# Optimization experiments

Measured on AMD Instinct MI355X. Metric: run time of the kernel, lower is better.

The kernel has to match this reference:

```python
import jax, jax.numpy as jnp
import numpy as np

NUM_GROUPS = 512   # G: number of FPS centers
GROUP_SIZE = 32    # K: neighbors per group


def setup_inputs() -> dict:
    key = jax.random.key(0)
    points = jax.random.normal(key, (16, 8192, 6), dtype=jnp.float32)  # [B,N,C], xyz = first 3 ch
    return {"points": points}


def _farthest_point_sampling(xyz, K):
    """Iterative FPS. xyz: [B,N,3] -> indices [B,K] (int32).

    Deterministic start at index 0 (the torch module uses a random start; we fix
    it for a reproducible reference -- the math per step is identical).
    """
    B, N, _ = xyz.shape
    start = jnp.zeros((B,), dtype=jnp.int32)
    min_d = jnp.full((B, N), jnp.inf, dtype=xyz.dtype)

    def step(carry, _):
        min_d, last = carry
        last_pt = jnp.take_along_axis(xyz, last[:, None, None], axis=1)  # [B,1,3]
        d = jnp.sum((xyz - last_pt) ** 2, axis=-1)                       # [B,N]
        min_d = jnp.minimum(min_d, d)
        nxt = jnp.argmax(min_d, axis=-1).astype(jnp.int32)
        return (min_d, nxt), last

    _, idxs = jax.lax.scan(step, (min_d, start), None, length=K)
    return jnp.transpose(idxs)  # [B,K]


def reference(points):
    xyz = points[:, :, :3]                                   # [B,N,3]
    fps_idx = _farthest_point_sampling(xyz, NUM_GROUPS)      # [B,G]
    centers = jnp.take_along_axis(xyz, fps_idx[:, :, None], axis=1)  # [B,G,3]

    # Squared pairwise distances [B,G,N] via expanded GEMM (compute-dominant part).
    d2 = (jnp.sum(centers * centers, axis=-1)[:, :, None]
          - 2.0 * jnp.einsum('bgc,bnc->bgn', centers, xyz)
          + jnp.sum(xyz * xyz, axis=-1)[:, None, :])

    # KNN: smallest K distances (torch uses return_sorted=False; ordering of the
    # K neighbors is irrelevant to the grouping semantics).
    _, knn_idx = jax.lax.top_k(-d2, GROUP_SIZE)              # [B,G,K]

    # knn_gather: [B,N,C] gathered by [B,G,K] -> [B,G,K,C]
    grouped = jax.vmap(lambda p, i: p[i])(points, knn_idx)

    # Center-subtract on xyz channels only.
    grouped = jnp.concatenate(
        [grouped[..., :3] - centers[:, :, None, :], grouped[..., 3:]], axis=-1)
    return grouped, centers
```

## Files before the change

### kernel.cpp

```cpp
#include <hip/hip_runtime.h>
#include <hip/hip_bf16.h>
#include <stdint.h>

#define BATCH 16
#define NPTS  8192
#define NCH   6
#define NGRP  512
#define GSZ   32

#define TPB    1024
#define FPS_PPT 8
#define FPS_W   16
#define GPB     4
#define KNB     (BATCH * NGRP / GPB)

typedef float v2f __attribute__((ext_vector_type(2)));

template <int CTRL>
__device__ __forceinline__ float dpp_max_f32(float v) {
  const int t =
      __builtin_amdgcn_update_dpp(0, __float_as_int(v), CTRL, 0xf, 0xf, true);
  return fmaxf(v, __int_as_float(t));
}

template <int CTRL>
__device__ __forceinline__ unsigned dpp_min_u32(unsigned v) {
  const int t = __builtin_amdgcn_update_dpp((int)0xFFFFFFFF, (int)v, CTRL,
                                            0xf, 0xf, false);
  const unsigned tu = (unsigned)t;
  return v < tu ? v : tu;
}

__global__ __launch_bounds__(TPB, 1) void fused_kernel(
    const float* __restrict__ points, float* __restrict__ grouped,
    float* __restrict__ centers, unsigned* __restrict__ ws) {
#pragma clang fp contract(off)
  __shared__ union {
    struct {
      float cache[NPTS * 3];
      unsigned long long wdata[2][FPS_W];
      unsigned wtag[2][FPS_W];
    } f;
    struct {
      unsigned long long wtop[16][GSZ];
      int knn_sh[GPB][GSZ];
    } k;
  } u;
  __shared__ unsigned ticket_sh;

  const int tid  = threadIdx.x;
  const int lane = tid & 63;
  const int wave = tid >> 6;

  if (tid == 0) ticket_sh = atomicAdd(ws, 1u);
  __syncthreads();
  const unsigned ticket = ticket_sh;

  if (ticket < BATCH) {
    const int b = (int)ticket;
    const float* P = points + (size_t)b * NPTS * NCH;
    float* C = centers + (size_t)b * NGRP * 3;
    unsigned* prog = ws + 32 + b * 32;

    v2f px[4], py[4], pz[4], md[4];
    {
      float* fx = (float*)px; float* fy = (float*)py; float* fz = (float*)pz;
#pragma unroll
      for (int j = 0; j < FPS_PPT; ++j) {
        const int i = tid * FPS_PPT + j;
        const float x = P[i * 6 + 0];
        const float y = P[i * 6 + 1];
        const float z = P[i * 6 + 2];
        fx[j] = x; fy[j] = y; fz[j] = z;
        u.f.cache[i * 3 + 0] = x;
        u.f.cache[i * 3 + 1] = y;
        u.f.cache[i * 3 + 2] = z;
      }
#pragma unroll
      for (int j = 0; j < 4; ++j)
        md[j] = (v2f){__builtin_inff(), __builtin_inff()};
    }
    if (tid < 32) u.f.wtag[tid >> 4][tid & 15] = 0;
    __syncthreads();

    float lx = u.f.cache[0], ly = u.f.cache[1], lz = u.f.cache[2];

    for (int k = 1; k < NGRP; ++k) {
      if (tid == 0) {
        if ((k & 7) == 0)
          __hip_atomic_store(prog, (unsigned)(k - 1), __ATOMIC_RELEASE,
                             __HIP_MEMORY_SCOPE_AGENT);
        C[(k - 1) * 3 + 0] = lx;
        C[(k - 1) * 3 + 1] = ly;
        C[(k - 1) * 3 + 2] = lz;
      }

      const v2f vlx = {lx, lx}, vly = {ly, ly}, vlz = {lz, lz};
      v2f b2 = {-__builtin_inff(), -__builtin_inff()};
#pragma unroll
      for (int j = 0; j < 4; ++j) {
        const v2f dx = px[j] - vlx;
        const v2f dy = py[j] - vly;
        const v2f dz = pz[j] - vlz;
        const v2f d  = (dx * dx + dy * dy) + dz * dz;
        md[j] = __builtin_elementwise_min(md[j], d);
        b2 = __builtin_elementwise_max(b2, md[j]);
      }
      const float bestv = fmaxf(b2.x, b2.y);

      unsigned idxbest = 0;
#pragma unroll
      for (int j = 3; j >= 0; --j) {
        idxbest = (md[j].y == bestv) ? (unsigned)(tid * 8 + 2 * j + 1) : idxbest;
        idxbest = (md[j].x == bestv) ? (unsigned)(tid * 8 + 2 * j)     : idxbest;
      }

      float wv = bestv;
      wv = dpp_max_f32<0x111>(wv); wv = dpp_max_f32<0x112>(wv);
      wv = dpp_max_f32<0x114>(wv); wv = dpp_max_f32<0x118>(wv);
      wv = dpp_max_f32<0x142>(wv); wv = dpp_max_f32<0x143>(wv);
      const float wvmax =
          __int_as_float(__builtin_amdgcn_readlane(__float_as_int(wv), 63));
      const int owner = (int)__builtin_ctzll(__ballot(bestv == wvmax));

      const int p = k & 1;
      if (lane == owner) {
        __hip_atomic_store(&u.f.wdata[p][wave],
                           ((unsigned long long)__float_as_uint(wvmax) << 32) |
                               idxbest,
                           __ATOMIC_RELAXED, __HIP_MEMORY_SCOPE_WORKGROUP);
        __hip_atomic_store(&u.f.wtag[p][wave], (unsigned)k, __ATOMIC_RELEASE,
                           __HIP_MEMORY_SCOPE_WORKGROUP);
      }

      unsigned tg;
      do {
        tg = __hip_atomic_load(&u.f.wtag[p][lane & 15], __ATOMIC_ACQUIRE,
                               __HIP_MEMORY_SCOPE_WORKGROUP);
      } while (__ballot(tg == (unsigned)k) != ~0ull);

      const unsigned long long slot =
          __hip_atomic_load(&u.f.wdata[p][lane & 15], __ATOMIC_RELAXED,
                            __HIP_MEMORY_SCOPE_WORKGROUP);
      const unsigned sidx = (unsigned)(slot & 0xFFFFFFFFull);
      const float    sval = __uint_as_float((unsigned)(slot >> 32));
      const float ccx = u.f.cache[sidx * 3 + 0];
      const float ccy = u.f.cache[sidx * 3 + 1];
      const float ccz = u.f.cache[sidx * 3 + 2];

      float r = sval;
      r = dpp_max_f32<0x111>(r); r = dpp_max_f32<0x112>(r);
      r = dpp_max_f32<0x114>(r); r = dpp_max_f32<0x118>(r);
      const float gmax =
          __int_as_float(__builtin_amdgcn_readlane(__float_as_int(r), 15));
      const int sstar =
          (int)__builtin_ctzll(__ballot(sval == gmax) & 0xFFFFull);
      lx = __int_as_float(__builtin_amdgcn_readlane(__float_as_int(ccx), sstar));
      ly = __int_as_float(__builtin_amdgcn_readlane(__float_as_int(ccy), sstar));
      lz = __int_as_float(__builtin_amdgcn_readlane(__float_as_int(ccz), sstar));
    }
    if (tid == 0) {
      C[(NGRP - 1) * 3 + 0] = lx;
      C[(NGRP - 1) * 3 + 1] = ly;
      C[(NGRP - 1) * 3 + 2] = lz;
      __hip_atomic_store(prog, (unsigned)NGRP, __ATOMIC_RELEASE,
                         __HIP_MEMORY_SCOPE_AGENT);
    }
  } else {
    const unsigned gid = ticket - BATCH;
    const int b  = (int)(gid & 15);
    const int g0 = (int)(gid >> 4) * GPB;
    const int sub  = tid >> 8;
    const int t256 = tid & 255;
    const int g = g0 + sub;
    const float* P = points + (size_t)b * NPTS * NCH;
    const float* cen = centers + ((size_t)b * NGRP + g) * 3;
    unsigned* prog = ws + 32 + b * 32;

    if (tid == 0) {
      while (__hip_atomic_load(prog, __ATOMIC_ACQUIRE,
                               __HIP_MEMORY_SCOPE_AGENT) <
             (unsigned)(g0 + GPB))
        __builtin_amdgcn_s_sleep(64);
    }
    __syncthreads();

    const float cx = __hip_atomic_load(&cen[0], __ATOMIC_RELAXED,
                                       __HIP_MEMORY_SCOPE_AGENT);
    const float cy = __hip_atomic_load(&cen[1], __ATOMIC_RELAXED,
                                       __HIP_MEMORY_SCOPE_AGENT);
    const float cz = __hip_atomic_load(&cen[2], __ATOMIC_RELAXED,
                                       __HIP_MEMORY_SCOPE_AGENT);
    const float cc = (cx * cx + cy * cy) + cz * cz;

    unsigned long long keys[32];
#pragma unroll
    for (int j = 0; j < 32; ++j) {
      const int i = j * 256 + t256;
      const float2 xy = *reinterpret_cast<const float2*>(P + (size_t)i * 6);
      const float x = xy.x, y = xy.y;
      const float z = P[i * 6 + 2];
      const float xx  = (x * x + y * y) + z * z;
      const float dot = fmaf(cz, z, fmaf(cy, y, cx * x));
      const float d2  = (cc - 2.0f * dot) + xx;
      unsigned uu = __float_as_uint(d2);
      uu = (uu & 0x80000000u) ? ~uu : (uu | 0x80000000u);
      keys[j] = ((unsigned long long)uu << 32) | (unsigned long long)(unsigned)i;
    }

    unsigned long long gm[4];
#pragma unroll
    for (int g2 = 0; g2 < 4; ++g2) {
      unsigned long long m = keys[g2 * 8];
#pragma unroll
      for (int t = 1; t < 8; ++t) {
        const unsigned long long o = keys[g2 * 8 + t];
        m = m < o ? m : o;
      }
      gm[g2] = m;
    }
    unsigned long long lmin;
    {
      const unsigned long long a2 = gm[0] < gm[1] ? gm[0] : gm[1];
      const unsigned long long b3 = gm[2] < gm[3] ? gm[2] : gm[3];
      lmin = a2 < b3 ? a2 : b3;
    }

    for (int r2 = 0; r2 < GSZ; ++r2) {
      const unsigned vcur = (unsigned)(lmin >> 32);
      const unsigned icur = (unsigned)(lmin & 0xFFFFFFFFull);
      unsigned vm = vcur;
      vm = dpp_min_u32<0x111>(vm); vm = dpp_min_u32<0x112>(vm);
      vm = dpp_min_u32<0x114>(vm); vm = dpp_min_u32<0x118>(vm);
      vm = dpp_min_u32<0x142>(vm); vm = dpp_min_u32<0x143>(vm);
      const unsigned vmin = (unsigned)__builtin_amdgcn_readlane((int)vm, 63);

      const unsigned long long mask = __ballot(vcur == vmin);
      unsigned imin;
      if (__builtin_popcountll(mask) == 1) {
        imin = (unsigned)__builtin_amdgcn_readlane(
            (int)icur, (int)__builtin_ctzll(mask));
      } else {
        unsigned ic = (vcur == vmin) ? icur : 0xFFFFFFFFu;
        ic = dpp_min_u32<0x111>(ic); ic = dpp_min_u32<0x112>(ic);
        ic = dpp_min_u32<0x114>(ic); ic = dpp_min_u32<0x118>(ic);
        ic = dpp_min_u32<0x142>(ic); ic = dpp_min_u32<0x143>(ic);
        imin = (unsigned)__builtin_amdgcn_readlane((int)ic, 63);
      }
      const unsigned long long wk =
          ((unsigned long long)vmin << 32) | (unsigned long long)imin;

      if (lane == (int)(imin & 63u)) {
#pragma unroll
        for (int g2 = 0; g2 < 4; ++g2) {
          if (gm[g2] == wk) {
            unsigned long long m = ~0ull;
#pragma unroll
            for (int t = 0; t < 8; ++t) {
              const int s = g2 * 8 + t;
              if (keys[s] == wk) keys[s] = ~0ull;
              const unsigned long long o = keys[s];
              m = m < o ? m : o;
            }
            gm[g2] = m;
          }
        }
        const unsigned long long a2 = gm[0] < gm[1] ? gm[0] : gm[1];
        const unsigned long long b3 = gm[2] < gm[3] ? gm[2] : gm[3];
        lmin = a2 < b3 ? a2 : b3;
      }
      if (lane == 0) u.k.wtop[wave][r2] = wk;
    }
    __syncthreads();

    if ((wave & 3) == 0) {
      const unsigned long long* flat = &u.k.wtop[4 * sub][0];
      unsigned long long a = flat[lane];
      unsigned long long c = flat[lane + 64];
#pragma unroll
      for (int k2 = 2; k2 <= 128; k2 <<= 1) {
#pragma unroll
        for (int j2 = k2 >> 1; j2 >= 1; j2 >>= 1) {
          if (j2 == 64) {
            const unsigned long long mn = a < c ? a : c;
            const unsigned long long mx = a < c ? c : a;
            a = mn; c = mx;
          } else {
            const bool upa = ((lane & k2) == 0);
            const bool upc = (((lane + 64) & k2) == 0);
            const unsigned long long oa = __shfl_xor(a, j2);
            const unsigned long long oc = __shfl_xor(c, j2);
            const bool low = ((lane & j2) == 0);
            const unsigned long long mna = a < oa ? a : oa;
            const unsigned long long mxa = a < oa ? oa : a;
            const unsigned long long mnc = c < oc ? c : oc;
            const unsigned long long mxc = c < oc ? oc : c;
            a = (low == upa) ? mna : mxa;
            c = (low == upc) ? mnc : mxc;
          }
        }
      }
      if (lane < GSZ) u.k.knn_sh[sub][lane] = (int)(unsigned)(a & 0xFFFFFFFFull);
    }
    __syncthreads();

    float* outg = grouped + ((size_t)b * NGRP + g) * GSZ * NCH;
    if (t256 < GSZ * NCH) {
      const int n = t256 / 6, c2 = t256 % 6;
      const int idx = u.k.knn_sh[sub][n];
      float v = P[idx * 6 + c2];
      if (c2 < 3) {
        const float cv = (c2 == 0) ? cx : (c2 == 1) ? cy : cz;
        v = v - cv;
      }
      outg[t256] = v;
    }
  }
}

extern "C" void kernel_launch(void* const* d_in, const int* in_sizes, int n_in,
                              void* d_out, int out_size, void* d_ws, size_t ws_size,
                              hipStream_t stream) {
  const float* points = (const float*)d_in[0];
  float* out = (float*)d_out;
  float* grouped = out;
  float* centers = out + (size_t)BATCH * NGRP * GSZ * NCH;
  unsigned* ws = (unsigned*)d_ws;

  hipMemsetAsync(ws, 0, 4096, stream);
  fused_kernel<<<BATCH + KNB, TPB, 0, stream>>>(points, grouped, centers, ws);
}
```

Measured before the change: 738.3 us.

## Run FPS with 8 waves, 16 points per thread, carry coordinates in wave slots

```diff
diff --git a/kernel.cpp b/kernel.cpp
--- a/kernel.cpp
+++ b/kernel.cpp
@@ -8,13 +8,15 @@
 #define NGRP  512
 #define GSZ   32
 
-#define TPB    1024
-#define FPS_PPT 8
-#define FPS_W   16
+#define TPB     1024
+#define FPS_TPB 512
+#define FPS_PPT 16
+#define FPS_W   8
 #define GPB     4
 #define KNB     (BATCH * NGRP / GPB)
 
 typedef float v2f __attribute__((ext_vector_type(2)));
+typedef float v4f __attribute__((ext_vector_type(4)));
 
 template <int CTRL>
 __device__ __forceinline__ float dpp_max_f32(float v) {
@@ -35,10 +37,10 @@
     const float* __restrict__ points, float* __restrict__ grouped,
     float* __restrict__ centers, unsigned* __restrict__ ws) {
 #pragma clang fp contract(off)
-  __shared__ union {
+  __shared__ __align__(16) union {
     struct {
-      float cache[NPTS * 3];
-      unsigned long long wdata[2][FPS_W];
+      float cache[NPTS * 4];
+      float wdata[2][FPS_W][4];
       unsigned wtag[2][FPS_W];
     } f;
     struct {
@@ -62,28 +64,36 @@
     float* C = centers + (size_t)b * NGRP * 3;
     unsigned* prog = ws + 32 + b * 32;
 
-    v2f px[4], py[4], pz[4], md[4];
+#pragma unroll
+    for (int j = 0; j < 8; ++j) {
+      const int i = tid * 8 + j;
+      const float2 xy = *reinterpret_cast<const float2*>(P + (size_t)i * 6);
+      const float z = P[i * 6 + 2];
+      v4f c4;
+      c4.x = xy.x; c4.y = xy.y; c4.z = z; c4.w = 0.0f;
+      *reinterpret_cast<v4f*>(&u.f.cache[i * 4]) = c4;
+    }
+    if (tid < 2 * FPS_W) u.f.wtag[tid >> 3][tid & 7] = 0;
+    __syncthreads();
+    if (tid >= FPS_TPB) return;
+
+    v2f px[8], py[8], pz[8], md[8];
+#pragma unroll
+    for (int m = 0; m < 8; ++m) {
+      const v4f a =
+          *reinterpret_cast<const v4f*>(&u.f.cache[(tid * FPS_PPT + 2 * m) * 4]);
+      const v4f bb = *reinterpret_cast<const v4f*>(
+          &u.f.cache[(tid * FPS_PPT + 2 * m + 1) * 4]);
+      px[m] = (v2f){a.x, bb.x};
+      py[m] = (v2f){a.y, bb.y};
+      pz[m] = (v2f){a.z, bb.z};
+      md[m] = (v2f){__builtin_inff(), __builtin_inff()};
+    }
+    float lx, ly, lz;
     {
-      float* fx = (float*)px; float* fy = (float*)py; float* fz = (float*)pz;
-#pragma unroll
-      for (int j = 0; j < FPS_PPT; ++j) {
-        const int i = tid * FPS_PPT + j;
-        const float x = P[i * 6 + 0];
-        const float y = P[i * 6 + 1];
-        const float z = P[i * 6 + 2];
-        fx[j] = x; fy[j] = y; fz[j] = z;
-        u.f.cache[i * 3 + 0] = x;
-        u.f.cache[i * 3 + 1] = y;
-        u.f.cache[i * 3 + 2] = z;
-      }
-#pragma unroll
-      for (int j = 0; j < 4; ++j)
-        md[j] = (v2f){__builtin_inff(), __builtin_inff()};
-    }
-    if (tid < 32) u.f.wtag[tid >> 4][tid & 15] = 0;
-    __syncthreads();
-
-    float lx = u.f.cache[0], ly = u.f.cache[1], lz = u.f.cache[2];
+      const v4f c0 = *reinterpret_cast<const v4f*>(&u.f.cache[0]);
+      lx = c0.x; ly = c0.y; lz = c0.z;
+    }
 
     for (int k = 1; k < NGRP; ++k) {
       if (tid == 0) {
@@ -98,22 +108,34 @@
       const v2f vlx = {lx, lx}, vly = {ly, ly}, vlz = {lz, lz};
       v2f b2 = {-__builtin_inff(), -__builtin_inff()};
 #pragma unroll
-      for (int j = 0; j < 4; ++j) {
-        const v2f dx = px[j] - vlx;
-        const v2f dy = py[j] - vly;
-        const v2f dz = pz[j] - vlz;
+      for (int m = 0; m < 8; ++m) {
+        const v2f dx = px[m] - vlx;
+        const v2f dy = py[m] - vly;
+        const v2f dz = pz[m] - vlz;
         const v2f d  = (dx * dx + dy * dy) + dz * dz;
-        md[j] = __builtin_elementwise_min(md[j], d);
-        b2 = __builtin_elementwise_max(b2, md[j]);
+        md[m] = __builtin_elementwise_min(md[m], d);
+        b2 = __builtin_elementwise_max(b2, md[m]);
       }
       const float bestv = fmaxf(b2.x, b2.y);
 
-      unsigned idxbest = 0;
-#pragma unroll
-      for (int j = 3; j >= 0; --j) {
-        idxbest = (md[j].y == bestv) ? (unsigned)(tid * 8 + 2 * j + 1) : idxbest;
-        idxbest = (md[j].x == bestv) ? (unsigned)(tid * 8 + 2 * j)     : idxbest;
-      }
+      unsigned cnd[8];
+#pragma unroll
+      for (int m = 0; m < 8; ++m) {
+        unsigned cm = (md[m].y == bestv) ? (unsigned)(2 * m + 1) : 0xFFFFFFFFu;
+        cm = (md[m].x == bestv) ? (unsigned)(2 * m) : cm;
+        cnd[m] = cm;
+      }
+      const unsigned m01 = cnd[0] < cnd[1] ? cnd[0] : cnd[1];
+      const unsigned m23 = cnd[2] < cnd[3] ? cnd[2] : cnd[3];
+      const unsigned m45 = cnd[4] < cnd[5] ? cnd[4] : cnd[5];
+      const unsigned m67 = cnd[6] < cnd[7] ? cnd[6] : cnd[7];
+      const unsigned m03 = m01 < m23 ? m01 : m23;
+      const unsigned m47 = m45 < m67 ? m45 : m67;
+      const unsigned cmin = m03 < m47 ? m03 : m47;
+      const unsigned idxbest = (unsigned)tid * FPS_PPT + cmin;
+
+      const v4f cg =
+          *reinterpret_cast<const v4f*>(&u.f.cache[idxbest * 4]);
 
       float wv = bestv;
       wv = dpp_max_f32<0x111>(wv); wv = dpp_max_f32<0x112>(wv);
@@ -125,39 +147,31 @@
 
       const int p = k & 1;
       if (lane == owner) {
-        __hip_atomic_store(&u.f.wdata[p][wave],
-                           ((unsigned long long)__float_as_uint(wvmax) << 32) |
-                               idxbest,
-                           __ATOMIC_RELAXED, __HIP_MEMORY_SCOPE_WORKGROUP);
+        v4f s;
+        s.x = wvmax; s.y = cg.x; s.z = cg.y; s.w = cg.z;
+        *reinterpret_cast<v4f*>(&u.f.wdata[p][wave][0]) = s;
         __hip_atomic_store(&u.f.wtag[p][wave], (unsigned)k, __ATOMIC_RELEASE,
                            __HIP_MEMORY_SCOPE_WORKGROUP);
       }
 
       unsigned tg;
       do {
-        tg = __hip_atomic_load(&u.f.wtag[p][lane & 15], __ATOMIC_ACQUIRE,
+        tg = __hip_atomic_load(&u.f.wtag[p][lane & 7], __ATOMIC_ACQUIRE,
                                __HIP_MEMORY_SCOPE_WORKGROUP);
       } while (__ballot(tg == (unsigned)k) != ~0ull);
 
-      const unsigned long long slot =
-          __hip_atomic_load(&u.f.wdata[p][lane & 15], __ATOMIC_RELAXED,
-                            __HIP_MEMORY_SCOPE_WORKGROUP);
-      const unsigned sidx = (unsigned)(slot & 0xFFFFFFFFull);
-      const float    sval = __uint_as_float((unsigned)(slot >> 32));
-      const float ccx = u.f.cache[sidx * 3 + 0];
-      const float ccy = u.f.cache[sidx * 3 + 1];
-      const float ccz = u.f.cache[sidx * 3 + 2];
-
-      float r = sval;
+      const v4f sl =
+          *reinterpret_cast<const v4f*>(&u.f.wdata[p][lane & 7][0]);
+      float r = sl.x;
       r = dpp_max_f32<0x111>(r); r = dpp_max_f32<0x112>(r);
-      r = dpp_max_f32<0x114>(r); r = dpp_max_f32<0x118>(r);
+      r = dpp_max_f32<0x114>(r);
       const float gmax =
-          __int_as_float(__builtin_amdgcn_readlane(__float_as_int(r), 15));
+          __int_as_float(__builtin_amdgcn_readlane(__float_as_int(r), 7));
       const int sstar =
-          (int)__builtin_ctzll(__ballot(sval == gmax) & 0xFFFFull);
-      lx = __int_as_float(__builtin_amdgcn_readlane(__float_as_int(ccx), sstar));
-      ly = __int_as_float(__builtin_amdgcn_readlane(__float_as_int(ccy), sstar));
-      lz = __int_as_float(__builtin_amdgcn_readlane(__float_as_int(ccz), sstar));
+          (int)__builtin_ctzll(__ballot(sl.x == gmax) & 0xFFull);
+      lx = __int_as_float(__builtin_amdgcn_readlane(__float_as_int(sl.y), sstar));
+      ly = __int_as_float(__builtin_amdgcn_readlane(__float_as_int(sl.z), sstar));
+      lz = __int_as_float(__builtin_amdgcn_readlane(__float_as_int(sl.w), sstar));
     }
     if (tid == 0) {
       C[(NGRP - 1) * 3 + 0] = lx;
```

Result: faster. 690.7 us (-6.5%).
